# Kernel optimization log

Hardware: AMD Instinct MI355X
Metric: run time of the kernel (lower is better)

## Reference

```python
import jax, jax.numpy as jnp
import numpy as np
import math

B, N, CS, CZ, H, HD, PQ, PV = 1, 512, 1024, 128, 12, 16, 4, 8
INF, EPS = 1e5, 1e-8


def _quat_to_rot(q):
    q = q / jnp.linalg.norm(q, axis=-1, keepdims=True)
    w, x, y, z = q[..., 0], q[..., 1], q[..., 2], q[..., 3]
    R = jnp.stack([
        1 - 2 * (y * y + z * z), 2 * (x * y - w * z), 2 * (x * z + w * y),
        2 * (x * y + w * z), 1 - 2 * (x * x + z * z), 2 * (y * z - w * x),
        2 * (x * z - w * y), 2 * (y * z + w * x), 1 - 2 * (x * x + y * y)
    ], axis=-1)
    return R.reshape(q.shape[:-1] + (3, 3))


def _split3(x):
    # torch.split into 3 chunks along last dim, then stack on new last dim
    d = x.shape[-1] // 3
    return jnp.stack((x[..., :d], x[..., d:2 * d], x[..., 2 * d:]), axis=-1)


def setup_inputs():
    key = jax.random.key(0)
    ks = jax.random.split(key, 12)

    def lin(k, din, dout):
        kw, kb = jax.random.split(k)
        W = jax.random.normal(kw, (din, dout), jnp.float32) / np.float32(np.sqrt(din))
        b = jax.random.normal(kb, (dout,), jnp.float32) * 0.01
        return W, b

    s = jax.random.normal(ks[0], (B, N, CS), jnp.float32)
    z = jax.random.normal(ks[1], (B, N, N, CZ), jnp.float32)
    rot = _quat_to_rot(jax.random.normal(ks[2], (B, N, 4), jnp.float32))
    trans = jax.random.normal(ks[3], (B, N, 3), jnp.float32) * 10.0
    mask = jnp.ones((B, N), jnp.float32)

    Wq, bq = lin(ks[4], CS, H * HD)
    Wkv, bkv = lin(ks[5], CS, 2 * H * HD)
    Wqp, bqp = lin(ks[6], CS, H * PQ * 3)
    Wkvp, bkvp = lin(ks[7], CS, H * (PQ + PV) * 3)
    Wb, bb = lin(ks[8], CZ, H)
    head_w = jax.random.normal(ks[9], (H,), jnp.float32) * 0.5
    Wout, bout = lin(ks[10], H * (CZ + HD + PV * 4), CS)

    return dict(s=s, z=z, rot=rot, trans=trans, mask=mask,
                Wq=Wq, bq=bq, Wkv=Wkv, bkv=bkv, Wqp=Wqp, bqp=bqp,
                Wkvp=Wkvp, bkvp=bkvp, Wb=Wb, bb=bb, head_w=head_w,
                Wout=Wout, bout=bout)


def _ipa(s, z, rot, trans, mask, Wq, bq, Wkv, bkv, Wqp, bqp, Wkvp, bkvp, Wb, bb, head_w, Wout, bout):
    # scalar q, k, v : [B, N, H, HD]
    q = (s @ Wq + bq).reshape(B, N, H, HD)
    kv = (s @ Wkv + bkv).reshape(B, N, H, 2 * HD)
    k, v = kv[..., :HD], kv[..., HD:]

    # point q/k/v in global frame: p' = R p + t
    q_pts = _split3(s @ Wqp + bqp)                      # [B, N, H*PQ, 3]
    q_pts = jnp.einsum('bnij,bnpj->bnpi', rot, q_pts) + trans[:, :, None, :]
    q_pts = q_pts.reshape(B, N, H, PQ, 3)

    kv_pts = _split3(s @ Wkvp + bkvp)                   # [B, N, H*(PQ+PV), 3]
    kv_pts = jnp.einsum('bnij,bnpj->bnpi', rot, kv_pts) + trans[:, :, None, :]
    kv_pts = kv_pts.reshape(B, N, H, PQ + PV, 3)
    k_pts, v_pts = kv_pts[..., :PQ, :], kv_pts[..., PQ:, :]

    # pair bias [B, N, N, H]
    b = z @ Wb + bb

    # scalar attention logits [B, H, N, N]
    a = jnp.einsum('bihd,bjhd->bhij', q, k) * np.float32(math.sqrt(1.0 / (3 * HD)))
    a = a + np.float32(math.sqrt(1.0 / 3)) * jnp.transpose(b, (0, 3, 1, 2))

    # point-distance attention: [B, N, N, H, PQ]
    diff = q_pts[:, :, None] - k_pts[:, None]           # [B, N, N, H, PQ, 3]
    pt_att = jnp.sum(diff * diff, axis=-1)
    hw = jax.nn.softplus(head_w) * np.float32(math.sqrt(1.0 / (3 * (PQ * 9.0 / 2))))
    pt_att = jnp.sum(pt_att * hw[:, None], axis=-1) * (-0.5)   # [B, N, N, H]
    a = a + jnp.transpose(pt_att, (0, 3, 1, 2))

    square_mask = INF * (mask[:, :, None] * mask[:, None, :] - 1.0)  # [B, N, N]
    a = jax.nn.softmax(a + square_mask[:, None], axis=-1)            # [B, H, N, N]

    # scalar output [B, N, H*HD]
    o = jnp.einsum('bhij,bjhd->bihd', a, v).reshape(B, N, H * HD)

    # point output, back to local frame: R^T (p - t)
    o_pt = jnp.einsum('bhij,bjhpc->bihpc', a, v_pts)                 # [B, N, H, PV, 3]
    o_pt = jnp.einsum('bnji,bnhpj->bnhpi', rot, o_pt - trans[:, :, None, None, :])
    o_pt_norm = jnp.sqrt(jnp.sum(o_pt * o_pt, axis=-1) + EPS).reshape(B, N, H * PV)
    o_pt_r = o_pt.reshape(B, N, H * PV, 3)

    # pair output [B, N, H*CZ]
    o_pair = jnp.einsum('bhij,bijc->bihc', a, z).reshape(B, N, H * CZ)

    cat = jnp.concatenate(
        (o, o_pt_r[..., 0], o_pt_r[..., 1], o_pt_r[..., 2], o_pt_norm, o_pair), axis=-1)
    return cat @ Wout + bout


def reference(s, z, rot, trans, mask, Wq, bq, Wkv, bkv, Wqp, bqp, Wkvp, bkvp, Wb, bb, head_w, Wout, bout):
    return _ipa(s, z, rot, trans, mask, Wq, bq, Wkv, bkv, Wqp, bqp, Wkvp, bkvp, Wb, bb, head_w, Wout, bout)
```

## Files before the change

kernel.cpp:

```cpp
#include <hip/hip_runtime.h>
#include <hip/hip_bf16.h>

#define N 512
#define CS 1024
#define CZ 128
#define H 12
#define HD 16

__device__ int sniff_f32(const unsigned short* p) {
    int bad = 0;
    for (int i = 0; i < 32; ++i) {
        unsigned short u = p[i];
        int e = (u >> 7) & 0xFF;
        if (e == 0xFF || e >= 141 || (e <= 27 && (u & 0x7FFFu) != 0)) bad++;
    }
    return bad > 0;
}

__device__ __forceinline__ float ld(const void* p, int i, int f32) {
    return f32 ? ((const float*)p)[i]
               : __bfloat162float(((const __hip_bfloat16*)p)[i]);
}

__device__ __forceinline__ float bfu(unsigned short u) {
    return __bfloat162float(*(const __hip_bfloat16*)&u);
}

typedef __attribute__((ext_vector_type(8))) short bf16x8;
typedef __attribute__((ext_vector_type(4))) float f32x4;
typedef __attribute__((ext_vector_type(4))) unsigned short u16x4;
typedef __attribute__((ext_vector_type(8))) unsigned short u16x8;

#define FG_LDA 40

__device__ __forceinline__ unsigned int split_bf16(float x) {
    __hip_bfloat16 hb = __float2bfloat16(x);
    float hf = __bfloat162float(hb);
    __hip_bfloat16 lb = __float2bfloat16(x - hf);
    unsigned int h = *reinterpret_cast<unsigned short*>(&hb);
    unsigned int l = *reinterpret_cast<unsigned short*>(&lb);
    return h | (l << 16);
}

__device__ __forceinline__ void wcat_resolve(int col,
        const void* Wq, const void* Wkv, const void* Wqp, const void* Wkvp,
        const void*& W, int& cc, int& ldim) {
    if (col < 192)      { W = Wq;   cc = col;       ldim = 192; }
    else if (col < 576) { W = Wkv;  cc = col - 192; ldim = 384; }
    else if (col < 720) { W = Wqp;  cc = col - 576; ldim = 144; }
    else                { W = Wkvp; cc = col - 720; ldim = 432; }
}

__global__ void proj_gemm(const void* s,
                          const void* Wq, const void* Wkv,
                          const void* Wqp, const void* Wkvp,
                          float* rawP)
{
    __shared__ unsigned short Ah[32][FG_LDA], Al[32][FG_LDA];
    __shared__ unsigned short Bh[64][FG_LDA], Bl[64][FG_LDA];
    __shared__ int flag;
    int t = threadIdx.x;
    int bn = blockIdx.x;
    int bm = blockIdx.y;
    if (t == 0) flag = sniff_f32((const unsigned short*)s);
    __syncthreads();
    int f32 = flag;

    int w  = t >> 6, l = t & 63;
    int wm = w >> 1, wn = w & 1;
    int lr = l & 15, lq = l >> 4;

    int am = t >> 3, aq = t & 7;
    int bc = t >> 2, bq = t & 3;

    const void* Wsrc; int wcc, wld;
    wcat_resolve(bn * 64 + bc, Wq, Wkv, Wqp, Wkvp, Wsrc, wcc, wld);

    f32x4 acc0 = {0.f, 0.f, 0.f, 0.f};
    f32x4 acc1 = {0.f, 0.f, 0.f, 0.f};

    int arowbase = (bm * 32 + am) * CS;

    for (int kt = 0; kt < CS / 32; ++kt) {
        {
            int base = arowbase + kt * 32 + aq * 4;
            u16x4 hh, ll;
            #pragma unroll
            for (int e = 0; e < 4; ++e) {
                unsigned int pe = split_bf16(ld(s, base + e, f32));
                hh[e] = (unsigned short)pe; ll[e] = (unsigned short)(pe >> 16);
            }
            *(u16x4*)&Ah[am][aq * 4] = hh;
            *(u16x4*)&Al[am][aq * 4] = ll;
        }
        {
            int kbase = kt * 32 + bq * 8;
            u16x8 hh, ll;
            #pragma unroll
            for (int e = 0; e < 8; ++e) {
                unsigned int pe = split_bf16(ld(Wsrc, (kbase + e) * wld + wcc, f32));
                hh[e] = (unsigned short)pe; ll[e] = (unsigned short)(pe >> 16);
            }
            *(u16x8*)&Bh[bc][bq * 8] = hh;
            *(u16x8*)&Bl[bc][bq * 8] = ll;
        }
        __syncthreads();
        bf16x8 a_h = *(const bf16x8*)&Ah[wm * 16 + lr][lq * 8];
        bf16x8 a_l = *(const bf16x8*)&Al[wm * 16 + lr][lq * 8];
        bf16x8 b0h = *(const bf16x8*)&Bh[wn * 32 + lr][lq * 8];
        bf16x8 b0l = *(const bf16x8*)&Bl[wn * 32 + lr][lq * 8];
        bf16x8 b1h = *(const bf16x8*)&Bh[wn * 32 + 16 + lr][lq * 8];
        bf16x8 b1l = *(const bf16x8*)&Bl[wn * 32 + 16 + lr][lq * 8];
        acc0 = __builtin_amdgcn_mfma_f32_16x16x32_bf16(a_h, b0h, acc0, 0, 0, 0);
        acc0 = __builtin_amdgcn_mfma_f32_16x16x32_bf16(a_h, b0l, acc0, 0, 0, 0);
        acc0 = __builtin_amdgcn_mfma_f32_16x16x32_bf16(a_l, b0h, acc0, 0, 0, 0);
        acc1 = __builtin_amdgcn_mfma_f32_16x16x32_bf16(a_h, b1h, acc1, 0, 0, 0);
        acc1 = __builtin_amdgcn_mfma_f32_16x16x32_bf16(a_h, b1l, acc1, 0, 0, 0);
        acc1 = __builtin_amdgcn_mfma_f32_16x16x32_bf16(a_l, b1h, acc1, 0, 0, 0);
        __syncthreads();
    }

    int col0 = bn * 64 + wn * 32 + lr;
    int row0 = bm * 32 + wm * 16 + lq * 4;
    #pragma unroll
    for (int r = 0; r < 4; ++r) {
        rawP[(row0 + r) * 1152 + col0]      = acc0[r];
        rawP[(row0 + r) * 1152 + col0 + 16] = acc1[r];
    }
}

__global__ void proj_post(const float* rawP,
                          const void* bq, const void* bkv,
                          const void* bqp, const void* bkvp,
                          const void* rot, const void* trans, const void* s,
                          float* q, float* kT, float* v,
                          float* qp, float* kpT, float* vp)
{
    __shared__ float rawL[576];
    __shared__ float R[9], T[3];
    __shared__ int flag;
    int t = threadIdx.x;
    int i = blockIdx.x;
    if (t == 0) flag = sniff_f32((const unsigned short*)s);
    __syncthreads();
    int f32 = flag;

    {
        float val = rawP[i * 1152 + t];
        if (t < 192) q[i * 192 + t] = val + ld(bq, t, f32);
        else {
            int cc = t - 192;
            float vv = val + ld(bkv, cc, f32);
            int h = cc >> 5, t2 = cc & 31;
            if (t2 < 16) kT[(h * 16 + t2) * 512 + i] = vv;
            else         v[i * 192 + h * 16 + (t2 - 16)] = vv;
        }
    }
    rawL[t] = rawP[i * 1152 + 576 + t]
            + (t < 144 ? ld(bqp, t, f32) : ld(bkvp, t - 144, f32));
    if (t < 9) R[t] = ld(rot, i * 9 + t, f32);
    if (t >= 16 && t < 19) T[t - 16] = ld(trans, i * 3 + (t - 16), f32);
    __syncthreads();
    if (t < 192) {
        float x, y, zc;
        if (t < 48) { x = rawL[t];        y = rawL[48 + t];   zc = rawL[96 + t]; }
        else { int pk = t - 48;
               x = rawL[144 + pk]; y = rawL[288 + pk]; zc = rawL[432 + pk]; }
        float rx = R[0]*x + R[1]*y + R[2]*zc + T[0];
        float ry = R[3]*x + R[4]*y + R[5]*zc + T[1];
        float rz = R[6]*x + R[7]*y + R[8]*zc + T[2];
        if (t < 48) {
            int h = t >> 2, pp = t & 3, b = i * 144 + h * 12 + pp * 3;
            qp[b] = rx; qp[b + 1] = ry; qp[b + 2] = rz;
        } else {
            int pk = t - 48, h = pk / 12, idx = pk % 12;
            if (idx < 4) {
                int row = h * 12 + idx * 3;
                kpT[(row + 0) * 512 + i] = rx;
                kpT[(row + 1) * 512 + i] = ry;
                kpT[(row + 2) * 512 + i] = rz;
            } else {
                int b = i * 288 + h * 24 + (idx - 4) * 3;
                vp[b] = rx; vp[b + 1] = ry; vp[b + 2] = rz;
            }
        }
    }
}

__global__ void attn_fused(const float* q, const float* kT, const float* v,
                           const float* qp, const float* kpT, const float* vp,
                           const void* z, const void* Wb, const void* bb,
                           const void* head_w, const void* mask,
                           const void* rot, const void* trans, const void* s,
                           float* cat)
{
    __shared__ float attL[H * N];
    __shared__ float WbL[CZ * H];
    __shared__ float U[6144];
    __shared__ float qL[192], qpL[144];
    __shared__ float RL[9], TL[3], bbL[H], hwL[H];
    __shared__ float miS;
    __shared__ int flag;
    int t = threadIdx.x;
    int i = blockIdx.x;
    if (t == 0) flag = sniff_f32((const unsigned short*)s);
    __syncthreads();
    int f32 = flag;
    for (int idx = t; idx < CZ * H; idx += 512) WbL[idx] = ld(Wb, idx, f32);
    if (t < 192) qL[t] = q[i * 192 + t];
    else if (t < 336) qpL[t - 192] = qp[i * 144 + (t - 192)];
    else if (t < 345) RL[t - 336] = ld(rot, i * 9 + (t - 336), f32);
    else if (t < 348) TL[t - 345] = ld(trans, i * 3 + (t - 345), f32);
    else if (t < 360) bbL[t - 348] = ld(bb, t - 348, f32);
    else if (t < 372) {
        float x = ld(head_w, t - 360, f32);
        float sp = (x > 20.f) ? x : log1pf(expf(x));
        hwL[t - 360] = sp * 0.13608276348795434f;
    }
    else if (t == 372) miS = ld(mask, i, f32);
    __syncthreads();

    {
        int jl = t >> 4, hs = t & 15;
        for (int jt = 0; jt < 16; ++jt) {
            __syncthreads();
            if (f32) {
                const float* zrow = (const float*)z + (i * N + jt * 32) * CZ;
                #pragma unroll
                for (int r = 0; r < 2; ++r) {
                    int flat = (t + 512 * r) * 4;
                    int row = flat >> 7, col = flat & 127;
                    float4 vz = *(const float4*)&zrow[flat];
                    *(float4*)&U[row * 132 + col] = vz;
                }
            } else {
                const unsigned short* zrow =
                    (const unsigned short*)z + (i * N + jt * 32) * CZ;
                int flat = t * 8;
                int row = flat >> 7, col = flat & 127;
                u16x8 uv = *(const u16x8*)&zrow[flat];
                float4 lo = {bfu(uv[0]), bfu(uv[1]), bfu(uv[2]), bfu(uv[3])};
                float4 hi = {bfu(uv[4]), bfu(uv[5]), bfu(uv[6]), bfu(uv[7])};
                *(float4*)&U[row * 132 + col] = lo;
                *(float4*)&U[row * 132 + col + 4] = hi;
            }
            __syncthreads();
            if (hs < H) {
                float acc = bbL[hs];
                #pragma unroll 8
                for (int c = 0; c < CZ; ++c)
                    acc += U[jl * 132 + c] * WbL[c * H + hs];
                attL[hs * N + jt * 32 + jl] = acc;
            }
        }
    }
    __syncthreads();

    {
        int j = t;
        float mj = ld(mask, j, f32);
        float mterm = 100000.0f * (miS * mj - 1.0f);
        const float* kTj  = kT + j;
        const float* kpTj = kpT + j;
        float bj[H];
        #pragma unroll
        for (int h = 0; h < H; ++h) bj[h] = attL[h * N + j];
        for (int h = 0; h < H; ++h) {
            float qk = 0.f;
            #pragma unroll
            for (int d = 0; d < 16; ++d)
                qk += qL[h * 16 + d] * kTj[(h * 16 + d) * 512];
            float pt = 0.f;
            #pragma unroll
            for (int p = 0; p < 4; ++p) {
                float dx = qpL[h*12 + p*3 + 0] - kpTj[(h*12 + p*3 + 0) * 512];
                float dy = qpL[h*12 + p*3 + 1] - kpTj[(h*12 + p*3 + 1) * 512];
                float dz = qpL[h*12 + p*3 + 2] - kpTj[(h*12 + p*3 + 2) * 512];
                pt += dx * dx + dy * dy + dz * dz;
            }
            attL[h * N + j] = qk * 0.14433756729740643f
                            + 0.5773502691896258f * bj[h]
                            - 0.5f * hwL[h] * pt + mterm;
        }
    }
    __syncthreads();

    {
        int w = t >> 6, l = t & 63;
        for (int h = w; h < H; h += 8) {
            float av[8];
            #pragma unroll
            for (int kk = 0; kk < 8; ++kk) av[kk] = attL[h * N + kk * 64 + l];
            float m = av[0];
            #pragma unroll
            for (int kk = 1; kk < 8; ++kk) m = fmaxf(m, av[kk]);
            for (int off = 1; off < 64; off <<= 1) m = fmaxf(m, __shfl_xor(m, off));
            float ssum = 0.f;
            #pragma unroll
            for (int kk = 0; kk < 8; ++kk) { av[kk] = __expf(av[kk] - m); ssum += av[kk]; }
            for (int off = 1; off < 64; off <<= 1) ssum += __shfl_xor(ssum, off);
            float inv = 1.0f / ssum;
            #pragma unroll
            for (int kk = 0; kk < 8; ++kk) attL[h * N + kk * 64 + l] = av[kk] * inv;
        }
    }
    __syncthreads();

    if (t < 192) {
        int h = t >> 4, d = t & 15;
        float acc = 0.f;
        for (int j = 0; j < N; ++j) acc += attL[h * N + j] * v[j * 192 + h * 16 + d];
        cat[i * 2112 + t] = acc;
    } else if (t < 288) {
        int hp = t - 192, h = hp >> 3, p = hp & 7;
        float ax = 0, ay = 0, az = 0;
        for (int j = 0; j < N; ++j) {
            float a_ = attL[h * N + j];
            int b2 = j * 288 + h * 24 + p * 3;
            ax += a_ * vp[b2]; ay += a_ * vp[b2 + 1]; az += a_ * vp[b2 + 2];
        }
        float gx = ax - TL[0], gy = ay - TL[1], gz = az - TL[2];
        float lx = RL[0]*gx + RL[3]*gy + RL[6]*gz;
        float ly = RL[1]*gx + RL[4]*gy + RL[7]*gz;
        float lz = RL[2]*gx + RL[5]*gy + RL[8]*gz;
        float nrm = sqrtf(lx*lx + ly*ly + lz*lz + 1e-8f);
        cat[i * 2112 + 192 + hp] = lx;
        cat[i * 2112 + 288 + hp] = ly;
        cat[i * 2112 + 384 + hp] = lz;
        cat[i * 2112 + 480 + hp] = nrm;
    }

    {
        int quarter = t >> 7, c = t & 127;
        float pacc[H];
        #pragma unroll
        for (int h = 0; h < H; ++h) pacc[h] = 0.f;
        int j0 = quarter * 128;
        if (f32) {
            const float* zp = (const float*)z + (i * N + j0) * CZ + c;
            for (int j = 0; j < 128; ++j) {
                float zc = zp[j * CZ];
                #pragma unroll
                for (int h = 0; h < H; ++h) pacc[h] += attL[h * N + j0 + j] * zc;
            }
        } else {
            const unsigned short* zp =
                (const unsigned short*)z + (i * N + j0) * CZ + c;
            for (int j = 0; j < 128; ++j) {
                float zc = bfu(zp[j * CZ]);
                #pragma unroll
                for (int h = 0; h < H; ++h) pacc[h] += attL[h * N + j0 + j] * zc;
            }
        }
        __syncthreads();
        #pragma unroll
        for (int h = 0; h < H; ++h) U[quarter * (H * CZ) + h * CZ + c] = pacc[h];
    }
    __syncthreads();
    for (int idx = t; idx < H * CZ; idx += 512)
        cat[i * 2112 + 576 + idx] =
            U[idx] + U[1536 + idx] + U[3072 + idx] + U[4608 + idx];
}

__global__ void final_gemm(const float* cat, const void* Wout, const void* bout,
                           void* out, const void* s)
{
    __shared__ unsigned short Ah[32][FG_LDA], Al[32][FG_LDA];
    __shared__ unsigned short Bh[64][FG_LDA], Bl[64][FG_LDA];
    __shared__ int flag;
    int t = threadIdx.x;
    int bn = blockIdx.x;
    int bm = blockIdx.y;
    if (t == 0) flag = sniff_f32((const unsigned short*)s);
    __syncthreads();
    int f32 = flag;

    int w  = t >> 6, l = t & 63;
    int wm = w >> 1, wn = w & 1;
    int lr = l & 15, lq = l >> 4;

    int am = t >> 3, aq = t & 7;
    int bc = t >> 2, bq = t & 3;

    f32x4 acc0 = {0.f, 0.f, 0.f, 0.f};
    f32x4 acc1 = {0.f, 0.f, 0.f, 0.f};

    const float* arow = &cat[(bm * 32 + am) * 2112];

    for (int kt = 0; kt < 2112 / 32; ++kt) {
        {
            float4 xv = *(const float4*)&arow[kt * 32 + aq * 4];
            unsigned int p0 = split_bf16(xv.x);
            unsigned int p1 = split_bf16(xv.y);
            unsigned int p2 = split_bf16(xv.z);
            unsigned int p3 = split_bf16(xv.w);
            u16x4 hh, ll;
            hh[0] = (unsigned short)p0; ll[0] = (unsigned short)(p0 >> 16);
            hh[1] = (unsigned short)p1; ll[1] = (unsigned short)(p1 >> 16);
            hh[2] = (unsigned short)p2; ll[2] = (unsigned short)(p2 >> 16);
            hh[3] = (unsigned short)p3; ll[3] = (unsigned short)(p3 >> 16);
            *(u16x4*)&Ah[am][aq * 4] = hh;
            *(u16x4*)&Al[am][aq * 4] = ll;
        }
        {
            int kbase = kt * 32 + bq * 8;
            u16x8 hh, ll;
            #pragma unroll
            for (int e = 0; e < 8; ++e) {
                float x = ld(Wout, (kbase + e) * CS + bn * 64 + bc, f32);
                unsigned int pe = split_bf16(x);
                hh[e] = (unsigned short)pe;
                ll[e] = (unsigned short)(pe >> 16);
            }
            *(u16x8*)&Bh[bc][bq * 8] = hh;
            *(u16x8*)&Bl[bc][bq * 8] = ll;
        }
        __syncthreads();
        bf16x8 a_h = *(const bf16x8*)&Ah[wm * 16 + lr][lq * 8];
        bf16x8 a_l = *(const bf16x8*)&Al[wm * 16 + lr][lq * 8];
        bf16x8 b0h = *(const bf16x8*)&Bh[wn * 32 + lr][lq * 8];
        bf16x8 b0l = *(const bf16x8*)&Bl[wn * 32 + lr][lq * 8];
        bf16x8 b1h = *(const bf16x8*)&Bh[wn * 32 + 16 + lr][lq * 8];
        bf16x8 b1l = *(const bf16x8*)&Bl[wn * 32 + 16 + lr][lq * 8];
        acc0 = __builtin_amdgcn_mfma_f32_16x16x32_bf16(a_h, b0h, acc0, 0, 0, 0);
        acc0 = __builtin_amdgcn_mfma_f32_16x16x32_bf16(a_h, b0l, acc0, 0, 0, 0);
        acc0 = __builtin_amdgcn_mfma_f32_16x16x32_bf16(a_l, b0h, acc0, 0, 0, 0);
        acc1 = __builtin_amdgcn_mfma_f32_16x16x32_bf16(a_h, b1h, acc1, 0, 0, 0);
        acc1 = __builtin_amdgcn_mfma_f32_16x16x32_bf16(a_h, b1l, acc1, 0, 0, 0);
        acc1 = __builtin_amdgcn_mfma_f32_16x16x32_bf16(a_l, b1h, acc1, 0, 0, 0);
        __syncthreads();
    }

    int col0 = bn * 64 + wn * 32 + lr;
    int row0 = bm * 32 + wm * 16 + lq * 4;
    float bv0 = ld(bout, col0, f32);
    float bv1 = ld(bout, col0 + 16, f32);
    if (f32) {
        float* o = (float*)out;
        #pragma unroll
        for (int r = 0; r < 4; ++r) {
            o[(row0 + r) * CS + col0]      = acc0[r] + bv0;
            o[(row0 + r) * CS + col0 + 16] = acc1[r] + bv1;
        }
    } else {
        __hip_bfloat16* o = (__hip_bfloat16*)out;
        #pragma unroll
        for (int r = 0; r < 4; ++r) {
            o[(row0 + r) * CS + col0]      = __float2bfloat16(acc0[r] + bv0);
            o[(row0 + r) * CS + col0 + 16] = __float2bfloat16(acc1[r] + bv1);
        }
    }
}

extern "C" void kernel_launch(void* const* d_in, const int* in_sizes, int n_in,
                              void* d_out, int out_size, void* d_ws, size_t ws_size,
                              hipStream_t stream)
{
    const void* s      = d_in[0];
    const void* z      = d_in[1];
    const void* rot    = d_in[2];
    const void* trans  = d_in[3];
    const void* mask   = d_in[4];
    const void* Wq     = d_in[5];  const void* bq   = d_in[6];
    const void* Wkv    = d_in[7];  const void* bkv  = d_in[8];
    const void* Wqp    = d_in[9];  const void* bqp  = d_in[10];
    const void* Wkvp   = d_in[11]; const void* bkvp = d_in[12];
    const void* Wb     = d_in[13]; const void* bb   = d_in[14];
    const void* head_w = d_in[15];
    const void* Wout   = d_in[16]; const void* bout = d_in[17];

    float* w    = (float*)d_ws;
    float* q    = w;
    float* kT   = q   + 98304;
    float* v    = kT  + 98304;
    float* qp   = v   + 98304;
    float* kpT  = qp  + 73728;
    float* vp   = kpT + 73728;
    float* cat  = vp  + 147456;
    float* rawP = cat;
    (void)ws_size; (void)in_sizes; (void)n_in; (void)out_size;

    proj_gemm <<<dim3(18, 16), 256, 0, stream>>>(s, Wq, Wkv, Wqp, Wkvp, rawP);
    proj_post <<<512, 576, 0, stream>>>(rawP, bq, bkv, bqp, bkvp, rot, trans, s,
                                        q, kT, v, qp, kpT, vp);
    attn_fused<<<512, 512, 0, stream>>>(q, kT, v, qp, kpT, vp, z, Wb, bb, head_w, mask,
                                        rot, trans, s, cat);
    final_gemm<<<dim3(16, 16), 256, 0, stream>>>(cat, Wout, bout, d_out, s);
}
```

Baseline: 457.2 us.

## Pre-split and transpose weights into bf16 hi/lo buffers, drop LDS staging in GEMMs

Adds a prep kernel that converts the projection weights and Wout into transposed bf16 high/low pairs in workspace. The two GEMMs then load MFMA operands straight from global memory, with no LDS tiles or barriers. The goal is to remove the strided, uncoalesced weight reads and the repeated per-block split_bf16 work. The cost is an extra kernel launch, more workspace traffic, and possibly poorer reuse now that shared memory no longer stages tiles.

```diff
diff --git a/kernel.cpp b/kernel.cpp
--- a/kernel.cpp
+++ b/kernel.cpp
@@ -6,6 +6,7 @@
 #define CZ 128
 #define H 12
 #define HD 16
+#define KC 2112
 
 __device__ int sniff_f32(const unsigned short* p) {
     int bad = 0;
@@ -28,10 +29,7 @@
 
 typedef __attribute__((ext_vector_type(8))) short bf16x8;
 typedef __attribute__((ext_vector_type(4))) float f32x4;
-typedef __attribute__((ext_vector_type(4))) unsigned short u16x4;
 typedef __attribute__((ext_vector_type(8))) unsigned short u16x8;
-
-#define FG_LDA 40
 
 __device__ __forceinline__ unsigned int split_bf16(float x) {
     __hip_bfloat16 hb = __float2bfloat16(x);
@@ -51,13 +49,62 @@
     else                { W = Wkvp; cc = col - 720; ldim = 432; }
 }
 
-__global__ void proj_gemm(const void* s,
-                          const void* Wq, const void* Wkv,
-                          const void* Wqp, const void* Wkvp,
-                          float* rawP)
+__global__ void prep_w(const void* Wq, const void* Wkv, const void* Wqp,
+                       const void* Wkvp, const void* Wout, const void* s,
+                       unsigned short* WcTh, unsigned short* WcTl,
+                       unsigned short* WoTh, unsigned short* WoTl)
 {
-    __shared__ unsigned short Ah[32][FG_LDA], Al[32][FG_LDA];
-    __shared__ unsigned short Bh[64][FG_LDA], Bl[64][FG_LDA];
+    __shared__ unsigned short th[32][33], tl[32][33];
+    __shared__ int flag;
+    int t = threadIdx.x;
+    if (t == 0) flag = sniff_f32((const unsigned short*)s);
+    __syncthreads();
+    int f32 = flag;
+    int tx = t & 31, ty = t >> 5;
+    int b = blockIdx.x;
+    if (b < 1152) {
+        int ct = b % 36, kt = b / 36;
+        int c0 = ct * 32, k0 = kt * 32;
+        #pragma unroll
+        for (int r = 0; r < 4; ++r) {
+            int k = k0 + ty + 8 * r, c = c0 + tx;
+            const void* W; int cc, ldim;
+            wcat_resolve(c, Wq, Wkv, Wqp, Wkvp, W, cc, ldim);
+            unsigned int pe = split_bf16(ld(W, k * ldim + cc, f32));
+            th[ty + 8 * r][tx] = (unsigned short)pe;
+            tl[ty + 8 * r][tx] = (unsigned short)(pe >> 16);
+        }
+        __syncthreads();
+        #pragma unroll
+        for (int r = 0; r < 4; ++r) {
+            int c = c0 + ty + 8 * r, k = k0 + tx;
+            WcTh[c * CS + k] = th[tx][ty + 8 * r];
+            WcTl[c * CS + k] = tl[tx][ty + 8 * r];
+        }
+    } else {
+        int bb = b - 1152;
+        int ct = bb & 31, kt = bb >> 5;
+        int c0 = ct * 32, k0 = kt * 32;
+        #pragma unroll
+        for (int r = 0; r < 4; ++r) {
+            int k = k0 + ty + 8 * r, c = c0 + tx;
+            unsigned int pe = split_bf16(ld(Wout, k * CS + c, f32));
+            th[ty + 8 * r][tx] = (unsigned short)pe;
+            tl[ty + 8 * r][tx] = (unsigned short)(pe >> 16);
+        }
+        __syncthreads();
+        #pragma unroll
+        for (int r = 0; r < 4; ++r) {
+            int c = c0 + ty + 8 * r, k = k0 + tx;
+            WoTh[c * KC + k] = th[tx][ty + 8 * r];
+            WoTl[c * KC + k] = tl[tx][ty + 8 * r];
+        }
+    }
+}
+
+__global__ void proj_gemm(const void* s, const unsigned short* BTh,
+                          const unsigned short* BTl, float* rawP)
+{
     __shared__ int flag;
     int t = threadIdx.x;
     int bn = blockIdx.x;
@@ -70,54 +117,42 @@
     int wm = w >> 1, wn = w & 1;
     int lr = l & 15, lq = l >> 4;
 
-    int am = t >> 3, aq = t & 7;
-    int bc = t >> 2, bq = t & 3;
-
-    const void* Wsrc; int wcc, wld;
-    wcat_resolve(bn * 64 + bc, Wq, Wkv, Wqp, Wkvp, Wsrc, wcc, wld);
+    int arow = bm * 32 + wm * 16 + lr;
+    int bcol = bn * 64 + wn * 32 + lr;
+    const unsigned short* bh = BTh + bcol * CS;
+    const unsigned short* bl = BTl + bcol * CS;
 
     f32x4 acc0 = {0.f, 0.f, 0.f, 0.f};
     f32x4 acc1 = {0.f, 0.f, 0.f, 0.f};
 
-    int arowbase = (bm * 32 + am) * CS;
-
+    #pragma unroll 2
     for (int kt = 0; kt < CS / 32; ++kt) {
-        {
-            int base = arowbase + kt * 32 + aq * 4;
-            u16x4 hh, ll;
-            #pragma unroll
-            for (int e = 0; e < 4; ++e) {
-                unsigned int pe = split_bf16(ld(s, base + e, f32));
-                hh[e] = (unsigned short)pe; ll[e] = (unsigned short)(pe >> 16);
-            }
-            *(u16x4*)&Ah[am][aq * 4] = hh;
-            *(u16x4*)&Al[am][aq * 4] = ll;
-        }
-        {
-            int kbase = kt * 32 + bq * 8;
-            u16x8 hh, ll;
+        int kk = kt * 32 + lq * 8;
+        u16x8 ah, al;
+        if (f32) {
+            const float* ap = (const float*)s + arow * CS + kk;
             #pragma unroll
             for (int e = 0; e < 8; ++e) {
-                unsigned int pe = split_bf16(ld(Wsrc, (kbase + e) * wld + wcc, f32));
-                hh[e] = (unsigned short)pe; ll[e] = (unsigned short)(pe >> 16);
-            }
-            *(u16x8*)&Bh[bc][bq * 8] = hh;
-            *(u16x8*)&Bl[bc][bq * 8] = ll;
-        }
-        __syncthreads();
-        bf16x8 a_h = *(const bf16x8*)&Ah[wm * 16 + lr][lq * 8];
-        bf16x8 a_l = *(const bf16x8*)&Al[wm * 16 + lr][lq * 8];
-        bf16x8 b0h = *(const bf16x8*)&Bh[wn * 32 + lr][lq * 8];
-        bf16x8 b0l = *(const bf16x8*)&Bl[wn * 32 + lr][lq * 8];
-        bf16x8 b1h = *(const bf16x8*)&Bh[wn * 32 + 16 + lr][lq * 8];
-        bf16x8 b1l = *(const bf16x8*)&Bl[wn * 32 + 16 + lr][lq * 8];
+                unsigned int pe = split_bf16(ap[e]);
+                ah[e] = (unsigned short)pe; al[e] = (unsigned short)(pe >> 16);
+            }
+        } else {
+            ah = *(const u16x8*)((const unsigned short*)s + arow * CS + kk);
+            #pragma unroll
+            for (int e = 0; e < 8; ++e) al[e] = 0;
+        }
+        bf16x8 b0h = *(const bf16x8*)(bh + kk);
+        bf16x8 b0l = *(const bf16x8*)(bl + kk);
+        bf16x8 b1h = *(const bf16x8*)(bh + 16 * CS + kk);
+        bf16x8 b1l = *(const bf16x8*)(bl + 16 * CS + kk);
+        bf16x8 a_h = *(bf16x8*)&ah;
+        bf16x8 a_l = *(bf16x8*)&al;
         acc0 = __builtin_amdgcn_mfma_f32_16x16x32_bf16(a_h, b0h, acc0, 0, 0, 0);
         acc0 = __builtin_amdgcn_mfma_f32_16x16x32_bf16(a_h, b0l, acc0, 0, 0, 0);
         acc0 = __builtin_amdgcn_mfma_f32_16x16x32_bf16(a_l, b0h, acc0, 0, 0, 0);
         acc1 = __builtin_amdgcn_mfma_f32_16x16x32_bf16(a_h, b1h, acc1, 0, 0, 0);
         acc1 = __builtin_amdgcn_mfma_f32_16x16x32_bf16(a_h, b1l, acc1, 0, 0, 0);
         acc1 = __builtin_amdgcn_mfma_f32_16x16x32_bf16(a_l, b1h, acc1, 0, 0, 0);
-        __syncthreads();
     }
 
     int col0 = bn * 64 + wn * 32 + lr;
@@ -362,11 +397,10 @@
             U[idx] + U[1536 + idx] + U[3072 + idx] + U[4608 + idx];
 }
 
-__global__ void final_gemm(const float* cat, const void* Wout, const void* bout,
+__global__ void final_gemm(const float* cat, const unsigned short* BTh,
+                           const unsigned short* BTl, const void* bout,
                            void* out, const void* s)
 {
-    __shared__ unsigned short Ah[32][FG_LDA], Al[32][FG_LDA];
-    __shared__ unsigned short Bh[64][FG_LDA], Bl[64][FG_LDA];
     __shared__ int flag;
     int t = threadIdx.x;
     int bn = blockIdx.x;
@@ -379,56 +413,37 @@
     int wm = w >> 1, wn = w & 1;
     int lr = l & 15, lq = l >> 4;
 
-    int am = t >> 3, aq = t & 7;
-    int bc = t >> 2, bq = t & 3;
+    int arow = bm * 32 + wm * 16 + lr;
+    int bcol = bn * 64 + wn * 32 + lr;
+    const unsigned short* bh = BTh + bcol * KC;
+    const unsigned short* bl = BTl + bcol * KC;
+    const float* ap0 = cat + arow * KC;
 
     f32x4 acc0 = {0.f, 0.f, 0.f, 0.f};
     f32x4 acc1 = {0.f, 0.f, 0.f, 0.f};
 
-    const float* arow = &cat[(bm * 32 + am) * 2112];
-
-    for (int kt = 0; kt < 2112 / 32; ++kt) {
-        {
-            float4 xv = *(const float4*)&arow[kt * 32 + aq * 4];
-            unsigned int p0 = split_bf16(xv.x);
-            unsigned int p1 = split_bf16(xv.y);
-            unsigned int p2 = split_bf16(xv.z);
-            unsigned int p3 = split_bf16(xv.w);
-            u16x4 hh, ll;
-            hh[0] = (unsigned short)p0; ll[0] = (unsigned short)(p0 >> 16);
-            hh[1] = (unsigned short)p1; ll[1] = (unsigned short)(p1 >> 16);
-            hh[2] = (unsigned short)p2; ll[2] = (unsigned short)(p2 >> 16);
-            hh[3] = (unsigned short)p3; ll[3] = (unsigned short)(p3 >> 16);
-            *(u16x4*)&Ah[am][aq * 4] = hh;
-            *(u16x4*)&Al[am][aq * 4] = ll;
-        }
-        {
-            int kbase = kt * 32 + bq * 8;
-            u16x8 hh, ll;
-            #pragma unroll
-            for (int e = 0; e < 8; ++e) {
-                float x = ld(Wout, (kbase + e) * CS + bn * 64 + bc, f32);
-                unsigned int pe = split_bf16(x);
-                hh[e] = (unsigned short)pe;
-                ll[e] = (unsigned short)(pe >> 16);
-            }
-            *(u16x8*)&Bh[bc][bq * 8] = hh;
-            *(u16x8*)&Bl[bc][bq * 8] = ll;
-        }
-        __syncthreads();
-        bf16x8 a_h = *(const bf16x8*)&Ah[wm * 16 + lr][lq * 8];
-        bf16x8 a_l = *(const bf16x8*)&Al[wm * 16 + lr][lq * 8];
-        bf16x8 b0h = *(const bf16x8*)&Bh[wn * 32 + lr][lq * 8];
-        bf16x8 b0l = *(const bf16x8*)&Bl[wn * 32 + lr][lq * 8];
-        bf16x8 b1h = *(const bf16x8*)&Bh[wn * 32 + 16 + lr][lq * 8];
-        bf16x8 b1l = *(const bf16x8*)&Bl[wn * 32 + 16 + lr][lq * 8];
+    #pragma unroll 2
+    for (int kt = 0; kt < KC / 32; ++kt) {
+        int kk = kt * 32 + lq * 8;
+        u16x8 ah, al;
+        const float* ap = ap0 + kk;
+        #pragma unroll
+        for (int e = 0; e < 8; ++e) {
+            unsigned int pe = split_bf16(ap[e]);
+            ah[e] = (unsigned short)pe; al[e] = (unsigned short)(pe >> 16);
+        }
+        bf16x8 b0h = *(const bf16x8*)(bh + kk);
+        bf16x8 b0l = *(const bf16x8*)(bl + kk);
+        bf16x8 b1h = *(const bf16x8*)(bh + 16 * KC + kk);
+        bf16x8 b1l = *(const bf16x8*)(bl + 16 * KC + kk);
+        bf16x8 a_h = *(bf16x8*)&ah;
+        bf16x8 a_l = *(bf16x8*)&al;
         acc0 = __builtin_amdgcn_mfma_f32_16x16x32_bf16(a_h, b0h, acc0, 0, 0, 0);
         acc0 = __builtin_amdgcn_mfma_f32_16x16x32_bf16(a_h, b0l, acc0, 0, 0, 0);
         acc0 = __builtin_amdgcn_mfma_f32_16x16x32_bf16(a_l, b0h, acc0, 0, 0, 0);
         acc1 = __builtin_amdgcn_mfma_f32_16x16x32_bf16(a_h, b1h, acc1, 0, 0, 0);
         acc1 = __builtin_amdgcn_mfma_f32_16x16x32_bf16(a_h, b1l, acc1, 0, 0, 0);
         acc1 = __builtin_amdgcn_mfma_f32_16x16x32_bf16(a_l, b1h, acc1, 0, 0, 0);
-        __syncthreads();
     }
 
     int col0 = bn * 64 + wn * 32 + lr;
@@ -478,12 +493,18 @@
     float* vp   = kpT + 73728;
     float* cat  = vp  + 147456;
     float* rawP = cat;
+    unsigned short* WcTh = (unsigned short*)(cat + 512 * 2112);
+    unsigned short* WcTl = WcTh + 1152 * 1024;
+    unsigned short* WoTh = WcTl + 1152 * 1024;
+    unsigned short* WoTl = WoTh + 1024 * 2112;
     (void)ws_size; (void)in_sizes; (void)n_in; (void)out_size;
 
-    proj_gemm <<<dim3(18, 16), 256, 0, stream>>>(s, Wq, Wkv, Wqp, Wkvp, rawP);
+    prep_w    <<<3264, 256, 0, stream>>>(Wq, Wkv, Wqp, Wkvp, Wout, s,
+                                         WcTh, WcTl, WoTh, WoTl);
+    proj_gemm <<<dim3(18, 16), 256, 0, stream>>>(s, WcTh, WcTl, rawP);
     proj_post <<<512, 576, 0, stream>>>(rawP, bq, bkv, bqp, bkvp, rot, trans, s,
                                         q, kT, v, qp, kpT, vp);
     attn_fused<<<512, 512, 0, stream>>>(q, kT, v, qp, kpT, vp, z, Wb, bb, head_w, mask,
                                         rot, trans, s, cat);
-    final_gemm<<<dim3(16, 16), 256, 0, stream>>>(cat, Wout, bout, d_out, s);
-}
+    final_gemm<<<dim3(16, 16), 256, 0, stream>>>(cat, WoTh, WoTl, bout, d_out, s);
+}
```

Result: faster. 435.2 us (-4.8%).
